# Kernel tuning notes

Measured on AMD Instinct MI355X. Metric: run time of the kernel, lower is better.

Reference implementation:

```python
import jax, jax.numpy as jnp
import numpy as np

N = 100000
H1, D1 = 8, 8          # conv1: 8 heads x 8 dims (concat -> 64)
C = 40                 # num_classes, conv2: 1 head
NEG_SLOPE = 0.2


def gat_layer(x, edge_index, W, a_src, a_dst, b, heads, out_dim, concat):
    # x: [N, F_in], W: [F_in, heads*out_dim], a_*: [heads, out_dim], b: [heads*out_dim] or [out_dim]
    h = (x @ W).reshape(-1, heads, out_dim)                 # [N, H, D]
    s_src = jnp.einsum('nhd,hd->nh', h, a_src)              # [N, H]
    s_dst = jnp.einsum('nhd,hd->nh', h, a_dst)              # [N, H]
    src, dst = edge_index[0], edge_index[1]
    e = jax.nn.leaky_relu(s_src[src] + s_dst[dst], NEG_SLOPE)   # [E, H]
    # segment softmax over incoming edges of each dst node
    m = jax.ops.segment_max(e, dst, num_segments=N)         # [N, H]
    e = jnp.exp(e - m[dst])
    z = jax.ops.segment_sum(e, dst, num_segments=N)         # [N, H]
    alpha = e / (z[dst] + 1e-16)                            # [E, H]
    msg = h[src] * alpha[:, :, None]                        # [E, H, D]
    out = jax.ops.segment_sum(msg, dst, num_segments=N)     # [N, H, D]
    if concat:
        out = out.reshape(-1, heads * out_dim)
    else:
        out = out.mean(axis=1)
    return out + b


def setup_inputs() -> dict:
    key = jax.random.key(0)
    ks = jax.random.split(key, 10)
    F_in = 256
    x = jax.random.normal(ks[0], (N, F_in), dtype=jnp.float32)
    edge_index = jax.random.randint(ks[1], (2, 1600000), 0, N, dtype=jnp.int32)
    sc1 = 1.0 / np.sqrt(F_in)
    W1 = jax.random.normal(ks[2], (F_in, H1 * D1), dtype=jnp.float32) * sc1
    a1_src = jax.random.normal(ks[3], (H1, D1), dtype=jnp.float32) * 0.1
    a1_dst = jax.random.normal(ks[4], (H1, D1), dtype=jnp.float32) * 0.1
    b1 = jnp.zeros((H1 * D1,), dtype=jnp.float32)
    sc2 = 1.0 / np.sqrt(H1 * D1)
    W2 = jax.random.normal(ks[5], (H1 * D1, C), dtype=jnp.float32) * sc2
    a2_src = jax.random.normal(ks[6], (1, C), dtype=jnp.float32) * 0.1
    a2_dst = jax.random.normal(ks[7], (1, C), dtype=jnp.float32) * 0.1
    b2 = jnp.zeros((C,), dtype=jnp.float32)
    return {"x": x, "edge_index": edge_index, "W1": W1, "a1_src": a1_src,
            "a1_dst": a1_dst, "b1": b1, "W2": W2, "a2_src": a2_src,
            "a2_dst": a2_dst, "b2": b2}


def reference(x, edge_index, W1, a1_src, a1_dst, b1, W2, a2_src, a2_dst, b2):
    # eval mode: dropout is identity
    h = gat_layer(x, edge_index, W1, a1_src, a1_dst, b1, H1, D1, concat=True)
    h = jax.nn.elu(h)
    out = gat_layer(h, edge_index, W2, a2_src, a2_dst, b2, 1, C, concat=False)
    return jax.nn.log_softmax(out, axis=1)
```

## Files before the change

### kernel.cpp

```cpp
#include <hip/hip_runtime.h>
#include <math.h>

#define BK 10
#define KNODES 1024
#define MAXNB 128

typedef __attribute__((ext_vector_type(8))) short bf16x8;
typedef __attribute__((ext_vector_type(4))) float f32x4;

__device__ __forceinline__ float bf2f(unsigned short u) {
  return __uint_as_float(((unsigned int)u) << 16);
}
__device__ __forceinline__ unsigned short f2bf(float f) {
  unsigned int i = __float_as_uint(f);
  unsigned int r = i + 0x7FFFu + ((i >> 16) & 1u);
  return (unsigned short)(r >> 16);
}

__global__ __launch_bounds__(256) void prep_kernel(
    const float* __restrict__ W1, const float* __restrict__ W2,
    const float* __restrict__ a2s, const float* __restrict__ a2d,
    unsigned short* __restrict__ whi, unsigned short* __restrict__ wlo,
    unsigned short* __restrict__ w2hi, unsigned short* __restrict__ w2lo,
    float* __restrict__ vas, float* __restrict__ vad,
    unsigned short* __restrict__ h1b, unsigned short* __restrict__ h2b,
    float* __restrict__ s1s, float* __restrict__ s2s,
    int* __restrict__ bpos, int capP, int NN) {
  const int blk = blockIdx.x, t = threadIdx.x;
  if (blk == 0 && t < MAXNB) bpos[t] = t * capP;
  if (blk < 32) {
    if (t < 64) {
      int b = blk, lane = t;
      int kt = b >> 2, ct = b & 3;
      int n = lane & 15, g = lane >> 4;
      unsigned short hb[8], lb[8];
#pragma unroll
      for (int j = 0; j < 8; ++j) {
        int k = kt * 32 + g * 8 + j;
        float wv = W1[k * 64 + ct * 16 + n];
        unsigned short hi = f2bf(wv);
        float rem = wv - bf2f(hi);
        hb[j] = hi;
        lb[j] = f2bf(rem);
      }
      size_t base = ((size_t)b * 64 + lane) * 8;
      *(ushort4*)(whi + base)     = make_ushort4(hb[0], hb[1], hb[2], hb[3]);
      *(ushort4*)(whi + base + 4) = make_ushort4(hb[4], hb[5], hb[6], hb[7]);
      *(ushort4*)(wlo + base)     = make_ushort4(lb[0], lb[1], lb[2], lb[3]);
      *(ushort4*)(wlo + base + 4) = make_ushort4(lb[4], lb[5], lb[6], lb[7]);
    }
  } else if (blk == 32) {
    if (t < 64) {
      float s = 0.f, d = 0.f;
      for (int c = 0; c < 40; ++c) {
        float w = W2[t * 40 + c];
        s += w * a2s[c];
        d += w * a2d[c];
      }
      vas[t] = s;
      vad[t] = d;
    }
  } else if (blk == 33) {
    if (t < 64) {
      h1b[(size_t)NN * 64 + t] = 0;
      if (t < 40) h2b[(size_t)NN * 40 + t] = 0;
      if (t < 8)  s1s[(size_t)NN * 8 + t] = -1e30f;
      if (t == 0) s2s[NN] = -1e30f;
    }
  } else if (blk >= 34 && blk < 40) {
    if (t < 64) {
      int b = blk - 34;
      int kt = b / 3, ct = b % 3;
      int n = t & 15, g = t >> 4;
      unsigned short hb[8], lb[8];
#pragma unroll
      for (int j = 0; j < 8; ++j) {
        int k = kt * 32 + g * 8 + j;
        int c = ct * 16 + n;
        float wv = (c < 40) ? W2[k * 40 + c] : 0.f;
        unsigned short hi = f2bf(wv);
        float rem = wv - bf2f(hi);
        hb[j] = hi;
        lb[j] = f2bf(rem);
      }
      size_t base = ((size_t)b * 64 + t) * 8;
      *(ushort4*)(w2hi + base)     = make_ushort4(hb[0], hb[1], hb[2], hb[3]);
      *(ushort4*)(w2hi + base + 4) = make_ushort4(hb[4], hb[5], hb[6], hb[7]);
      *(ushort4*)(w2lo + base)     = make_ushort4(lb[0], lb[1], lb[2], lb[3]);
      *(ushort4*)(w2lo + base + 4) = make_ushort4(lb[4], lb[5], lb[6], lb[7]);
    }
  }
}

__global__ __launch_bounds__(256) void gemm1_mfma_kernel(
    const float* __restrict__ x, const unsigned short* __restrict__ whi,
    const unsigned short* __restrict__ wlo,
    const float* __restrict__ a_src, const float* __restrict__ a_dst,
    unsigned short* __restrict__ h1b,
    float* __restrict__ s_src, float* __restrict__ s_dst, int N) {
  __shared__ float xtile[4][2048];
  const int w = threadIdx.x >> 6, lane = threadIdx.x & 63;
  const int m = lane & 15, g = lane >> 4;
  const int rbase = blockIdx.x * 64 + w * 16;
  float* xw = xtile[w];

  const int lrow2 = lane >> 5;
  const int lch   = lane & 31;
  const int msw   = m & 7;

  f32x4 acc[4] = {{0.f, 0.f, 0.f, 0.f}, {0.f, 0.f, 0.f, 0.f},
                  {0.f, 0.f, 0.f, 0.f}, {0.f, 0.f, 0.f, 0.f}};

#pragma unroll
  for (int half = 0; half < 2; ++half) {
    const int colbase = half * 128;
    if (half) asm volatile("s_waitcnt lgkmcnt(0)" ::: "memory");
#pragma unroll
    for (int j = 0; j < 8; ++j) {
      int lrow = 2 * j + lrow2;
      int row = rbase + lrow;
      if (row >= N) row = N - 1;
      int sw = lrow & 7;
      const float* src = x + (size_t)row * 256 + colbase + ((lch ^ sw) << 2);
      __builtin_amdgcn_global_load_lds(
          (const __attribute__((address_space(1))) unsigned int*)src,
          (__attribute__((address_space(3))) unsigned int*)(xw + j * 256),
          16, 0, 0);
    }
    asm volatile("s_waitcnt vmcnt(0)" ::: "memory");
#pragma unroll
    for (int ktl = 0; ktl < 4; ++ktl) {
      const int kt = half * 4 + ktl;
      const int c0 = ktl * 8 + g * 2;
      const float* p0 = xw + m * 128 + (((c0)     ^ msw) << 2);
      const float* p1 = xw + m * 128 + (((c0 + 1) ^ msw) << 2);
      float4 a0 = *(const float4*)p0;
      float4 a1 = *(const float4*)p1;
      float av[8] = {a0.x, a0.y, a0.z, a0.w, a1.x, a1.y, a1.z, a1.w};
      bf16x8 ahi, alo;
#pragma unroll
      for (int j = 0; j < 8; ++j) {
        unsigned int u = __float_as_uint(av[j]);
        unsigned short hi = (unsigned short)(u >> 16);
        float rem = av[j] - bf2f(hi);
        ahi[j] = (short)hi;
        alo[j] = (short)(__float_as_uint(rem) >> 16);
      }
      const unsigned short* wp = whi + ((size_t)(kt * 4) * 64 + lane) * 8;
      const unsigned short* lp = wlo + ((size_t)(kt * 4) * 64 + lane) * 8;
#pragma unroll
      for (int ct = 0; ct < 4; ++ct) {
        bf16x8 bh = *(const bf16x8*)(wp + (size_t)ct * 64 * 8);
        bf16x8 bl = *(const bf16x8*)(lp + (size_t)ct * 64 * 8);
        acc[ct] = __builtin_amdgcn_mfma_f32_16x16x32_bf16(ahi, bh, acc[ct], 0, 0, 0);
        acc[ct] = __builtin_amdgcn_mfma_f32_16x16x32_bf16(alo, bh, acc[ct], 0, 0, 0);
        acc[ct] = __builtin_amdgcn_mfma_f32_16x16x32_bf16(ahi, bl, acc[ct], 0, 0, 0);
      }
    }
  }
#pragma unroll
  for (int r = 0; r < 4; ++r) {
    int ro = rbase + g * 4 + r;
    if (ro < N) {
#pragma unroll
      for (int ct = 0; ct < 4; ++ct)
        h1b[(size_t)ro * 64 + ct * 16 + m] = f2bf(acc[ct][r]);
    }
  }
  float a1sv[4], a1dv[4];
#pragma unroll
  for (int ct = 0; ct < 4; ++ct) {
    a1sv[ct] = a_src[ct * 16 + m];
    a1dv[ct] = a_dst[ct * 16 + m];
  }
#pragma unroll
  for (int r = 0; r < 4; ++r) {
    float ps[4], pd[4];
#pragma unroll
    for (int ct = 0; ct < 4; ++ct) {
      ps[ct] = acc[ct][r] * a1sv[ct];
      pd[ct] = acc[ct][r] * a1dv[ct];
    }
#pragma unroll
    for (int off = 1; off < 8; off <<= 1) {
#pragma unroll
      for (int ct = 0; ct < 4; ++ct) {
        ps[ct] += __shfl_xor(ps[ct], off);
        pd[ct] += __shfl_xor(pd[ct], off);
      }
    }
    int ro = rbase + g * 4 + r;
    if ((m & 7) == 0 && ro < N) {
      int hb2 = m >> 3;
#pragma unroll
      for (int ct = 0; ct < 4; ++ct) {
        s_src[(size_t)ro * 8 + ct * 2 + hb2] = ps[ct];
        s_dst[(size_t)ro * 8 + ct * 2 + hb2] = pd[ct];
      }
    }
  }
}

__global__ __launch_bounds__(256) void bin_kernel(const int* __restrict__ src,
                                                  const int* __restrict__ dst,
                                                  int* __restrict__ bpos,
                                                  unsigned int* __restrict__ payload,
                                                  int E, int NB, int capP) {
  __shared__ int hist[MAXNB], soff[MAXNB], base[MAXNB], rnk[MAXNB];
  __shared__ unsigned int stage[4096];
  const int t = threadIdx.x;
  const int e0 = blockIdx.x * 4096;
  if (t < MAXNB) { hist[t] = 0; rnk[t] = 0; }
  __syncthreads();
  for (int j = t; j < 4096; j += 256) {
    int e = e0 + j;
    if (e < E) atomicAdd(&hist[dst[e] >> BK], 1);
  }
  __syncthreads();
  if (t == 0) {
    int acc = 0;
    for (int b = 0; b < NB; ++b) { soff[b] = acc; acc += hist[b]; }
  }
  __syncthreads();
  if (t < NB) {
    int c = hist[t];
    base[t] = c ? atomicAdd(&bpos[t], c) : 0;
  }
  __syncthreads();
  for (int j = t; j < 4096; j += 256) {
    int e = e0 + j;
    if (e < E) {
      int d = dst[e];
      int b = d >> BK;
      int s = src[e];
      int r = atomicAdd(&rnk[b], 1);
      stage[soff[b] + r] = (((unsigned)(d & (KNODES - 1))) << 17) | (unsigned)s;
    }
  }
  __syncthreads();
  int wave = t >> 6, lane = t & 63;
  for (int b = wave; b < NB; b += 4) {
    int len = hist[b], bs = soff[b], gb = base[b];
    int lim = (b + 1) * capP;
    for (int j = lane; j < len; j += 64)
      if (gb + j < lim) payload[gb + j] = stage[bs + j];
  }
}

__global__ __launch_bounds__(1024) void fill2_kernel(const unsigned int* __restrict__ payload,
                                                     const int* __restrict__ bpos,
                                                     int* __restrict__ col,
                                                     int* __restrict__ rbeg,
                                                     int* __restrict__ rend,
                                                     int capP, int NN) {
  __shared__ int cnt[KNODES], scn[KNODES], pos[KNODES];
  const int b = blockIdx.x, t = threadIdx.x;
  cnt[t] = 0;
  __syncthreads();
  const int beg = b * capP;
  int len = bpos[b] - beg;
  if (len > capP) len = capP;
  for (int j = t; j < len; j += 1024) atomicAdd(&cnt[payload[beg + j] >> 17], 1);
  __syncthreads();
  const int myc = cnt[t];
  const int padc = (myc + 7) & ~7;
  scn[t] = padc;
  __syncthreads();
  for (int off = 1; off < 1024; off <<= 1) {
    int v = (t >= off) ? scn[t - off] : 0;
    __syncthreads();
    scn[t] += v;
    __syncthreads();
  }
  const int mystart = b * (capP + 8 * KNODES) + scn[t] - padc;
  const int n = (b << BK) + t;
  if (n < NN) { rbeg[n] = mystart; rend[n] = mystart + padc; }
  pos[t] = mystart;
  __syncthreads();
  for (int j = t; j < len; j += 1024) {
    unsigned int pay = payload[beg + j];
    int p = atomicAdd(&pos[pay >> 17], 1);
    col[p] = (int)(pay & 0x1FFFF);
  }
  __syncthreads();
  for (int j = mystart + myc; j < mystart + padc; ++j) col[j] = NN;
}

__global__ __launch_bounds__(256) void agg1_kernel(
    const int* __restrict__ rbeg, const int* __restrict__ rend,
    const int* __restrict__ col,
    const float* __restrict__ s_src, const float* __restrict__ s_dst,
    const unsigned short* __restrict__ h1b, const float* __restrict__ b1,
    const float* __restrict__ vas, const float* __restrict__ vad,
    unsigned short* __restrict__ helub, float* __restrict__ s2s,
    float* __restrict__ s2d, int N) {
  int wv = threadIdx.x >> 6;
  int l  = threadIdx.x & 63;
  int n  = blockIdx.x * 4 + wv;
  if (n >= N) return;
  const int q  = l >> 3;
  const int hh = l & 7;
  const float sdq = s_dst[n * 8 + hh];
  const int beg = __builtin_amdgcn_readfirstlane(rbeg[n]);
  const int end = __builtin_amdgcn_readfirstlane(rend[n]);
  float z = 0.f, acc = 0.f, acc2 = 0.f;
  int e = beg;
  if (((end - beg) >> 3) & 1) {
    int4 ia = *(const int4*)(col + e);
    int4 ib = *(const int4*)(col + e + 4);
    int myidx = col[e + q];
    float pv = s_src[(unsigned)myidx * 8u + (unsigned)hh];
    float tt = pv + sdq;
    tt = fmaxf(tt, 0.2f * tt);
    float w = __expf(tt);
    z += w;
    int idxs[8] = {ia.x, ia.y, ia.z, ia.w, ib.x, ib.y, ib.z, ib.w};
#pragma unroll
    for (int j = 0; j < 8; ++j) {
      float wj = __shfl(w, j * 8 + q, 64);
      unsigned short g = h1b[(unsigned)idxs[j] * 64u + (unsigned)l];
      acc = fmaf(wj, bf2f(g), acc);
    }
    e += 8;
  }
  for (; e < end; e += 16) {
    int4 ia = *(const int4*)(col + e);
    int4 ib = *(const int4*)(col + e + 4);
    int4 ic = *(const int4*)(col + e + 8);
    int4 id = *(const int4*)(col + e + 12);
    int my0 = col[e + q];
    int my1 = col[e + 8 + q];
    float pv0 = s_src[(unsigned)my0 * 8u + (unsigned)hh];
    float pv1 = s_src[(unsigned)my1 * 8u + (unsigned)hh];
    int idxs[16] = {ia.x, ia.y, ia.z, ia.w, ib.x, ib.y, ib.z, ib.w,
                    ic.x, ic.y, ic.z, ic.w, id.x, id.y, id.z, id.w};
    unsigned short gg[16];
#pragma unroll
    for (int j = 0; j < 16; ++j) gg[j] = h1b[(unsigned)idxs[j] * 64u + (unsigned)l];
    float t0 = pv0 + sdq; t0 = fmaxf(t0, 0.2f * t0); float w0 = __expf(t0);
    float t1 = pv1 + sdq; t1 = fmaxf(t1, 0.2f * t1); float w1 = __expf(t1);
    z += w0 + w1;
#pragma unroll
    for (int j = 0; j < 8; ++j) {
      float wj = __shfl(w0, j * 8 + q, 64);
      acc = fmaf(wj, bf2f(gg[j]), acc);
    }
#pragma unroll
    for (int j = 0; j < 8; ++j) {
      float wj = __shfl(w1, j * 8 + q, 64);
      acc2 = fmaf(wj, bf2f(gg[8 + j]), acc2);
    }
  }
  acc += acc2;
  z += __shfl_xor(z, 8); z += __shfl_xor(z, 16); z += __shfl_xor(z, 32);
  float zf = __shfl(z, 9 * q, 64);
  float v = acc / (zf + 1e-16f) + b1[l];
  v = v > 0.f ? v : (__expf(v) - 1.f);
  helub[(size_t)n * 64 + l] = f2bf(v);
  float ps = v * vas[l];
  float pd = v * vad[l];
  for (int off = 32; off > 0; off >>= 1) {
    ps += __shfl_xor(ps, off);
    pd += __shfl_xor(pd, off);
  }
  if (l == 0) { s2s[n] = ps; s2d[n] = pd; }
}

__global__ __launch_bounds__(256) void gemm2_mfma_kernel(
    const unsigned short* __restrict__ heb, const unsigned short* __restrict__ w2hi,
    const unsigned short* __restrict__ w2lo, unsigned short* __restrict__ h2b, int N) {
  const int w = threadIdx.x >> 6, lane = threadIdx.x & 63;
  const int m = lane & 15, g = lane >> 4;
  const int rbase = blockIdx.x * 64 + w * 16;
  int arow = rbase + m;
  if (arow >= N) arow = N - 1;
  const unsigned short* hrow = heb + (size_t)arow * 64 + g * 8;
  f32x4 acc[3] = {{0.f, 0.f, 0.f, 0.f}, {0.f, 0.f, 0.f, 0.f}, {0.f, 0.f, 0.f, 0.f}};
#pragma unroll
  for (int kt = 0; kt < 2; ++kt) {
    bf16x8 a = *(const bf16x8*)(hrow + kt * 32);
#pragma unroll
    for (int ct = 0; ct < 3; ++ct) {
      int b = kt * 3 + ct;
      bf16x8 bh = *(const bf16x8*)(w2hi + ((size_t)b * 64 + lane) * 8);
      bf16x8 bl = *(const bf16x8*)(w2lo + ((size_t)b * 64 + lane) * 8);
      acc[ct] = __builtin_amdgcn_mfma_f32_16x16x32_bf16(a, bh, acc[ct], 0, 0, 0);
      acc[ct] = __builtin_amdgcn_mfma_f32_16x16x32_bf16(a, bl, acc[ct], 0, 0, 0);
    }
  }
#pragma unroll
  for (int r = 0; r < 4; ++r) {
    int ro = rbase + g * 4 + r;
    if (ro < N) {
#pragma unroll
      for (int ct = 0; ct < 3; ++ct) {
        int c = ct * 16 + m;
        if (c < 40) h2b[(size_t)ro * 40 + c] = f2bf(acc[ct][r]);
      }
    }
  }
}

__global__ __launch_bounds__(256) void agg2_kernel(
    const int* __restrict__ rbeg, const int* __restrict__ rend,
    const int* __restrict__ col,
    const float* __restrict__ s2s, const float* __restrict__ s2d,
    const unsigned short* __restrict__ h2b, const float* __restrict__ b2,
    float* __restrict__ out, int N) {
  int wv = threadIdx.x >> 6;
  int l  = threadIdx.x & 63;
  int n  = blockIdx.x * 4 + wv;
  if (n >= N) return;
  const int q = l >> 3;
  const bool act = (l < 40);
  const unsigned lc = act ? (unsigned)l : 0u;
  const float sdv = s2d[n];
  const int beg = __builtin_amdgcn_readfirstlane(rbeg[n]);
  const int end = __builtin_amdgcn_readfirstlane(rend[n]);
  float z = 0.f, acc = 0.f, acc2 = 0.f;
  int e = beg;
  if (((end - beg) >> 3) & 1) {
    int4 ia = *(const int4*)(col + e);
    int4 ib = *(const int4*)(col + e + 4);
    int myidx = col[e + q];
    float pv = s2s[myidx];
    float tt = pv + sdv;
    tt = fmaxf(tt, 0.2f * tt);
    float w = __expf(tt);
    z += w;
    int idxs[8] = {ia.x, ia.y, ia.z, ia.w, ib.x, ib.y, ib.z, ib.w};
#pragma unroll
    for (int j = 0; j < 8; ++j) {
      float wj = __shfl(w, j * 8, 64);
      unsigned short g = h2b[(unsigned)idxs[j] * 40u + lc];
      acc = fmaf(wj, bf2f(g), acc);
    }
    e += 8;
  }
  for (; e < end; e += 16) {
    int4 ia = *(const int4*)(col + e);
    int4 ib = *(const int4*)(col + e + 4);
    int4 ic = *(const int4*)(col + e + 8);
    int4 id = *(const int4*)(col + e + 12);
    int my0 = col[e + q];
    int my1 = col[e + 8 + q];
    float pv0 = s2s[my0];
    float pv1 = s2s[my1];
    int idxs[16] = {ia.x, ia.y, ia.z, ia.w, ib.x, ib.y, ib.z, ib.w,
                    ic.x, ic.y, ic.z, ic.w, id.x, id.y, id.z, id.w};
    unsigned short gg[16];
#pragma unroll
    for (int j = 0; j < 16; ++j) gg[j] = h2b[(unsigned)idxs[j] * 40u + lc];
    float t0 = pv0 + sdv; t0 = fmaxf(t0, 0.2f * t0); float w0 = __expf(t0);
    float t1 = pv1 + sdv; t1 = fmaxf(t1, 0.2f * t1); float w1 = __expf(t1);
    z += w0 + w1;
#pragma unroll
    for (int j = 0; j < 8; ++j) {
      float wj = __shfl(w0, j * 8, 64);
      acc = fmaf(wj, bf2f(gg[j]), acc);
    }
#pragma unroll
    for (int j = 0; j < 8; ++j) {
      float wj = __shfl(w1, j * 8, 64);
      acc2 = fmaf(wj, bf2f(gg[8 + j]), acc2);
    }
  }
  acc += acc2;
  z += __shfl_xor(z, 8); z += __shfl_xor(z, 16); z += __shfl_xor(z, 32);
  float v = act ? (acc / (z + 1e-16f) + b2[l]) : -1e30f;
  float m = v;
  for (int off = 32; off > 0; off >>= 1) m = fmaxf(m, __shfl_xor(m, off));
  float ex = act ? __expf(v - m) : 0.f;
  float s = ex;
  for (int off = 32; off > 0; off >>= 1) s += __shfl_xor(s, off);
  if (act) out[(size_t)n * 40 + l] = v - m - logf(s);
}

extern "C" void kernel_launch(void* const* d_in, const int* in_sizes, int n_in,
                              void* d_out, int out_size, void* d_ws, size_t ws_size,
                              hipStream_t stream) {
  const float* x   = (const float*)d_in[0];
  const int*   ei  = (const int*)d_in[1];
  const float* W1  = (const float*)d_in[2];
  const float* a1s = (const float*)d_in[3];
  const float* a1d = (const float*)d_in[4];
  const float* b1  = (const float*)d_in[5];
  const float* W2  = (const float*)d_in[6];
  const float* a2s = (const float*)d_in[7];
  const float* a2d = (const float*)d_in[8];
  const float* b2  = (const float*)d_in[9];
  float* out = (float*)d_out;
  (void)n_in; (void)out_size; (void)ws_size;

  const int NN = in_sizes[0] / 256;
  const int E  = in_sizes[1] / 2;
  const int NB = (NN + KNODES - 1) >> BK;
  const int* esrc = ei;
  const int* edst = ei + E;

  int capP = (E + NB - 1) / NB;
  capP += capP / 4 + capP / 16 + 512;
  capP = (capP + 15) & ~15;

  char* p = (char*)d_ws;
  auto alloc = [&](size_t bytes) -> char* {
    char* q = p;
    p += (bytes + 255) & ~(size_t)255;
    return q;
  };
  unsigned short* h1b   = (unsigned short*)alloc((size_t)(NN + 1) * 64 * 2);
  unsigned short* helub = (unsigned short*)alloc((size_t)NN * 64 * 2);
  unsigned short* h2b   = (unsigned short*)alloc((size_t)(NN + 1) * 40 * 2);
  float* s1s  = (float*)alloc((size_t)(NN + 1) * 8 * 4);
  float* s1d  = (float*)alloc((size_t)NN * 8 * 4);
  float* s2s  = (float*)alloc((size_t)(NN + 1) * 4);
  float* s2d  = (float*)alloc((size_t)NN * 4);
  int*   rbeg = (int*)alloc((size_t)NN * 4);
  int*   rend = (int*)alloc((size_t)NN * 4);
  int*   bpos = (int*)alloc(MAXNB * 4);
  unsigned int* payload = (unsigned int*)alloc((size_t)NB * capP * 4);
  int*   col  = (int*)alloc((size_t)NB * (capP + 8 * KNODES) * 4);
  float* vas  = (float*)alloc(64 * 4);
  float* vad  = (float*)alloc(64 * 4);
  unsigned short* w1hi = (unsigned short*)alloc(32 * 64 * 8 * 2);
  unsigned short* w1lo = (unsigned short*)alloc(32 * 64 * 8 * 2);
  unsigned short* w2hi = (unsigned short*)alloc(6 * 64 * 8 * 2);
  unsigned short* w2lo = (unsigned short*)alloc(6 * 64 * 8 * 2);

  prep_kernel<<<40, 256, 0, stream>>>(W1, W2, a2s, a2d, w1hi, w1lo, w2hi, w2lo,
                                      vas, vad, h1b, h2b, s1s, s2s, bpos, capP, NN);
  bin_kernel<<<(E + 4095) / 4096, 256, 0, stream>>>(esrc, edst, bpos, payload, E, NB, capP);
  fill2_kernel<<<NB, 1024, 0, stream>>>(payload, bpos, col, rbeg, rend, capP, NN);
  gemm1_mfma_kernel<<<(NN + 63) / 64, 256, 0, stream>>>(x, w1hi, w1lo, a1s, a1d,
                                                        h1b, s1s, s1d, NN);
  agg1_kernel<<<(NN + 3) / 4, 256, 0, stream>>>(rbeg, rend, col, s1s, s1d, h1b, b1,
                                                vas, vad, helub, s2s, s2d, NN);
  gemm2_mfma_kernel<<<(NN + 63) / 64, 256, 0, stream>>>(helub, w2hi, w2lo, h2b, NN);
  agg2_kernel<<<(NN + 3) / 4, 256, 0, stream>>>(rbeg, rend, col, s2s, s2d, h2b, b2, out, NN);
}
```

Before: 349.3 us.

## Fuse edge binning into GEMM1 launch and GEMM2 into layer-1 aggregation

Edge binning and the first-layer GEMM now run as one launch, with block roles interleaved and shared memory held in a union, so the two independent phases overlap on the device. The second-layer GEMM moves into the layer-1 aggregation kernel: each 512-thread block aggregates 8 nodes, stages the ELU outputs in LDS, and one wave runs the MFMA. This removes the helub intermediate round-trip through global memory and one launch. The fill kernel's block-wide Hillis-Steele scan is replaced by a wave-shuffle scan, cutting barriers. In exchange, only one wave per block does the MFMA work, on 8 of its 16 rows, and the larger blocks may lower occupancy in the aggregation kernel.

```diff
diff --git a/kernel.cpp b/kernel.cpp
--- a/kernel.cpp
+++ b/kernel.cpp
@@ -92,17 +92,79 @@
   }
 }
 
-__global__ __launch_bounds__(256) void gemm1_mfma_kernel(
+__global__ __launch_bounds__(256) void g1bin_kernel(
     const float* __restrict__ x, const unsigned short* __restrict__ whi,
     const unsigned short* __restrict__ wlo,
     const float* __restrict__ a_src, const float* __restrict__ a_dst,
     unsigned short* __restrict__ h1b,
-    float* __restrict__ s_src, float* __restrict__ s_dst, int N) {
-  __shared__ float xtile[4][2048];
+    float* __restrict__ s_src, float* __restrict__ s_dst, int N,
+    const int* __restrict__ esrc, const int* __restrict__ edst,
+    int* __restrict__ bpos, unsigned int* __restrict__ payload,
+    int E, int NB, int capP, int nG1, int nBin) {
+  __shared__ union {
+    float xtile[4][2048];
+    struct {
+      int hist[MAXNB], soff[MAXNB], base[MAXNB], rnk[MAXNB];
+      unsigned int stage[4096];
+    } b;
+  } sm;
+
+  const int bid = blockIdx.x;
+  int isBin, id;
+  if (2 * nBin <= nG1 + nBin) {
+    if (bid < 2 * nBin) { isBin = bid & 1; id = bid >> 1; }
+    else                { isBin = 0;       id = bid - nBin; }
+  } else {
+    isBin = (bid < nBin);
+    id = isBin ? bid : bid - nBin;
+  }
+
+  if (isBin) {
+    const int t = threadIdx.x;
+    const int e0 = id * 4096;
+    if (t < MAXNB) { sm.b.hist[t] = 0; sm.b.rnk[t] = 0; }
+    __syncthreads();
+    for (int j = t; j < 4096; j += 256) {
+      int e = e0 + j;
+      if (e < E) atomicAdd(&sm.b.hist[edst[e] >> BK], 1);
+    }
+    __syncthreads();
+    if (t == 0) {
+      int acc = 0;
+      for (int b = 0; b < NB; ++b) { sm.b.soff[b] = acc; acc += sm.b.hist[b]; }
+    }
+    __syncthreads();
+    if (t < NB) {
+      int c = sm.b.hist[t];
+      sm.b.base[t] = c ? atomicAdd(&bpos[t], c) : 0;
+    }
+    __syncthreads();
+    for (int j = t; j < 4096; j += 256) {
+      int e = e0 + j;
+      if (e < E) {
+        int d = edst[e];
+        int b = d >> BK;
+        int s = esrc[e];
+        int r = atomicAdd(&sm.b.rnk[b], 1);
+        sm.b.stage[sm.b.soff[b] + r] =
+            (((unsigned)(d & (KNODES - 1))) << 17) | (unsigned)s;
+      }
+    }
+    __syncthreads();
+    int wave = t >> 6, lane = t & 63;
+    for (int b = wave; b < NB; b += 4) {
+      int len = sm.b.hist[b], bs = sm.b.soff[b], gb = sm.b.base[b];
+      int lim = (b + 1) * capP;
+      for (int j = lane; j < len; j += 64)
+        if (gb + j < lim) payload[gb + j] = sm.b.stage[bs + j];
+    }
+    return;
+  }
+
   const int w = threadIdx.x >> 6, lane = threadIdx.x & 63;
   const int m = lane & 15, g = lane >> 4;
-  const int rbase = blockIdx.x * 64 + w * 16;
-  float* xw = xtile[w];
+  const int rbase = id * 64 + w * 16;
+  float* xw = sm.xtile[w];
 
   const int lrow2 = lane >> 5;
   const int lch   = lane & 31;
@@ -201,59 +263,14 @@
   }
 }
 
-__global__ __launch_bounds__(256) void bin_kernel(const int* __restrict__ src,
-                                                  const int* __restrict__ dst,
-                                                  int* __restrict__ bpos,
-                                                  unsigned int* __restrict__ payload,
-                                                  int E, int NB, int capP) {
-  __shared__ int hist[MAXNB], soff[MAXNB], base[MAXNB], rnk[MAXNB];
-  __shared__ unsigned int stage[4096];
-  const int t = threadIdx.x;
-  const int e0 = blockIdx.x * 4096;
-  if (t < MAXNB) { hist[t] = 0; rnk[t] = 0; }
-  __syncthreads();
-  for (int j = t; j < 4096; j += 256) {
-    int e = e0 + j;
-    if (e < E) atomicAdd(&hist[dst[e] >> BK], 1);
-  }
-  __syncthreads();
-  if (t == 0) {
-    int acc = 0;
-    for (int b = 0; b < NB; ++b) { soff[b] = acc; acc += hist[b]; }
-  }
-  __syncthreads();
-  if (t < NB) {
-    int c = hist[t];
-    base[t] = c ? atomicAdd(&bpos[t], c) : 0;
-  }
-  __syncthreads();
-  for (int j = t; j < 4096; j += 256) {
-    int e = e0 + j;
-    if (e < E) {
-      int d = dst[e];
-      int b = d >> BK;
-      int s = src[e];
-      int r = atomicAdd(&rnk[b], 1);
-      stage[soff[b] + r] = (((unsigned)(d & (KNODES - 1))) << 17) | (unsigned)s;
-    }
-  }
-  __syncthreads();
-  int wave = t >> 6, lane = t & 63;
-  for (int b = wave; b < NB; b += 4) {
-    int len = hist[b], bs = soff[b], gb = base[b];
-    int lim = (b + 1) * capP;
-    for (int j = lane; j < len; j += 64)
-      if (gb + j < lim) payload[gb + j] = stage[bs + j];
-  }
-}
-
 __global__ __launch_bounds__(1024) void fill2_kernel(const unsigned int* __restrict__ payload,
                                                      const int* __restrict__ bpos,
                                                      int* __restrict__ col,
                                                      int* __restrict__ rbeg,
                                                      int* __restrict__ rend,
                                                      int capP, int NN) {
-  __shared__ int cnt[KNODES], scn[KNODES], pos[KNODES];
+  __shared__ int cnt[KNODES], pos[KNODES];
+  __shared__ int wsum[16];
   const int b = blockIdx.x, t = threadIdx.x;
   cnt[t] = 0;
   __syncthreads();
@@ -264,15 +281,27 @@
   __syncthreads();
   const int myc = cnt[t];
   const int padc = (myc + 7) & ~7;
-  scn[t] = padc;
-  __syncthreads();
-  for (int off = 1; off < 1024; off <<= 1) {
-    int v = (t >= off) ? scn[t - off] : 0;
-    __syncthreads();
-    scn[t] += v;
-    __syncthreads();
-  }
-  const int mystart = b * (capP + 8 * KNODES) + scn[t] - padc;
+  const int lane = t & 63, wid = t >> 6;
+  int v = padc;
+#pragma unroll
+  for (int off = 1; off < 64; off <<= 1) {
+    int u = __shfl_up(v, off, 64);
+    if (lane >= off) v += u;
+  }
+  if (lane == 63) wsum[wid] = v;
+  __syncthreads();
+  if (t < 16) {
+    int sv = wsum[t];
+#pragma unroll
+    for (int off = 1; off < 16; off <<= 1) {
+      int u = __shfl_up(sv, off, 64);
+      if ((int)t >= off) sv += u;
+    }
+    wsum[t] = sv;
+  }
+  __syncthreads();
+  const int incl = v + (wid ? wsum[wid - 1] : 0);
+  const int mystart = b * (capP + 8 * KNODES) + incl - padc;
   const int n = (b << BK) + t;
   if (n < NN) { rbeg[n] = mystart; rend[n] = mystart + padc; }
   pos[t] = mystart;
@@ -286,116 +315,121 @@
   for (int j = mystart + myc; j < mystart + padc; ++j) col[j] = NN;
 }
 
-__global__ __launch_bounds__(256) void agg1_kernel(
+__global__ __launch_bounds__(512) void agg1_kernel(
     const int* __restrict__ rbeg, const int* __restrict__ rend,
     const int* __restrict__ col,
     const float* __restrict__ s_src, const float* __restrict__ s_dst,
     const unsigned short* __restrict__ h1b, const float* __restrict__ b1,
     const float* __restrict__ vas, const float* __restrict__ vad,
-    unsigned short* __restrict__ helub, float* __restrict__ s2s,
+    const unsigned short* __restrict__ w2hi, const unsigned short* __restrict__ w2lo,
+    unsigned short* __restrict__ h2b, float* __restrict__ s2s,
     float* __restrict__ s2d, int N) {
-  int wv = threadIdx.x >> 6;
-  int l  = threadIdx.x & 63;
-  int n  = blockIdx.x * 4 + wv;
-  if (n >= N) return;
-  const int q  = l >> 3;
-  const int hh = l & 7;
-  const float sdq = s_dst[n * 8 + hh];
-  const int beg = __builtin_amdgcn_readfirstlane(rbeg[n]);
-  const int end = __builtin_amdgcn_readfirstlane(rend[n]);
-  float z = 0.f, acc = 0.f, acc2 = 0.f;
-  int e = beg;
-  if (((end - beg) >> 3) & 1) {
-    int4 ia = *(const int4*)(col + e);
-    int4 ib = *(const int4*)(col + e + 4);
-    int myidx = col[e + q];
-    float pv = s_src[(unsigned)myidx * 8u + (unsigned)hh];
-    float tt = pv + sdq;
-    tt = fmaxf(tt, 0.2f * tt);
-    float w = __expf(tt);
-    z += w;
-    int idxs[8] = {ia.x, ia.y, ia.z, ia.w, ib.x, ib.y, ib.z, ib.w};
-#pragma unroll
-    for (int j = 0; j < 8; ++j) {
-      float wj = __shfl(w, j * 8 + q, 64);
-      unsigned short g = h1b[(unsigned)idxs[j] * 64u + (unsigned)l];
-      acc = fmaf(wj, bf2f(g), acc);
-    }
-    e += 8;
-  }
-  for (; e < end; e += 16) {
-    int4 ia = *(const int4*)(col + e);
-    int4 ib = *(const int4*)(col + e + 4);
-    int4 ic = *(const int4*)(col + e + 8);
-    int4 id = *(const int4*)(col + e + 12);
-    int my0 = col[e + q];
-    int my1 = col[e + 8 + q];
-    float pv0 = s_src[(unsigned)my0 * 8u + (unsigned)hh];
-    float pv1 = s_src[(unsigned)my1 * 8u + (unsigned)hh];
-    int idxs[16] = {ia.x, ia.y, ia.z, ia.w, ib.x, ib.y, ib.z, ib.w,
-                    ic.x, ic.y, ic.z, ic.w, id.x, id.y, id.z, id.w};
-    unsigned short gg[16];
-#pragma unroll
-    for (int j = 0; j < 16; ++j) gg[j] = h1b[(unsigned)idxs[j] * 64u + (unsigned)l];
-    float t0 = pv0 + sdq; t0 = fmaxf(t0, 0.2f * t0); float w0 = __expf(t0);
-    float t1 = pv1 + sdq; t1 = fmaxf(t1, 0.2f * t1); float w1 = __expf(t1);
-    z += w0 + w1;
-#pragma unroll
-    for (int j = 0; j < 8; ++j) {
-      float wj = __shfl(w0, j * 8 + q, 64);
-      acc = fmaf(wj, bf2f(gg[j]), acc);
-    }
-#pragma unroll
-    for (int j = 0; j < 8; ++j) {
-      float wj = __shfl(w1, j * 8 + q, 64);
-      acc2 = fmaf(wj, bf2f(gg[8 + j]), acc2);
-    }
-  }
-  acc += acc2;
-  z += __shfl_xor(z, 8); z += __shfl_xor(z, 16); z += __shfl_xor(z, 32);
-  float zf = __shfl(z, 9 * q, 64);
-  float v = acc / (zf + 1e-16f) + b1[l];
-  v = v > 0.f ? v : (__expf(v) - 1.f);
-  helub[(size_t)n * 64 + l] = f2bf(v);
-  float ps = v * vas[l];
-  float pd = v * vad[l];
-  for (int off = 32; off > 0; off >>= 1) {
-    ps += __shfl_xor(ps, off);
-    pd += __shfl_xor(pd, off);
-  }
-  if (l == 0) { s2s[n] = ps; s2d[n] = pd; }
-}
-
-__global__ __launch_bounds__(256) void gemm2_mfma_kernel(
-    const unsigned short* __restrict__ heb, const unsigned short* __restrict__ w2hi,
-    const unsigned short* __restrict__ w2lo, unsigned short* __restrict__ h2b, int N) {
-  const int w = threadIdx.x >> 6, lane = threadIdx.x & 63;
-  const int m = lane & 15, g = lane >> 4;
-  const int rbase = blockIdx.x * 64 + w * 16;
-  int arow = rbase + m;
-  if (arow >= N) arow = N - 1;
-  const unsigned short* hrow = heb + (size_t)arow * 64 + g * 8;
-  f32x4 acc[3] = {{0.f, 0.f, 0.f, 0.f}, {0.f, 0.f, 0.f, 0.f}, {0.f, 0.f, 0.f, 0.f}};
-#pragma unroll
-  for (int kt = 0; kt < 2; ++kt) {
-    bf16x8 a = *(const bf16x8*)(hrow + kt * 32);
-#pragma unroll
-    for (int ct = 0; ct < 3; ++ct) {
-      int b = kt * 3 + ct;
-      bf16x8 bh = *(const bf16x8*)(w2hi + ((size_t)b * 64 + lane) * 8);
-      bf16x8 bl = *(const bf16x8*)(w2lo + ((size_t)b * 64 + lane) * 8);
-      acc[ct] = __builtin_amdgcn_mfma_f32_16x16x32_bf16(a, bh, acc[ct], 0, 0, 0);
-      acc[ct] = __builtin_amdgcn_mfma_f32_16x16x32_bf16(a, bl, acc[ct], 0, 0, 0);
-    }
-  }
-#pragma unroll
-  for (int r = 0; r < 4; ++r) {
-    int ro = rbase + g * 4 + r;
-    if (ro < N) {
+  __shared__ float vsh[16][68];
+  const int t  = threadIdx.x;
+  const int wv = t >> 6;
+  const int l  = t & 63;
+  const int n  = blockIdx.x * 8 + wv;
+  const bool alive = (n < N);
+  float v = 0.f;
+  if (alive) {
+    const int q  = l >> 3;
+    const int hh = l & 7;
+    const float sdq = s_dst[n * 8 + hh];
+    const int beg = __builtin_amdgcn_readfirstlane(rbeg[n]);
+    const int end = __builtin_amdgcn_readfirstlane(rend[n]);
+    float z = 0.f, acc = 0.f, acc2 = 0.f;
+    int e = beg;
+    if (((end - beg) >> 3) & 1) {
+      int4 ia = *(const int4*)(col + e);
+      int4 ib = *(const int4*)(col + e + 4);
+      int myidx = col[e + q];
+      float pv = s_src[(unsigned)myidx * 8u + (unsigned)hh];
+      float tt = pv + sdq;
+      tt = fmaxf(tt, 0.2f * tt);
+      float ww = __expf(tt);
+      z += ww;
+      int idxs[8] = {ia.x, ia.y, ia.z, ia.w, ib.x, ib.y, ib.z, ib.w};
+#pragma unroll
+      for (int j = 0; j < 8; ++j) {
+        float wj = __shfl(ww, j * 8 + q, 64);
+        unsigned short gbit = h1b[(unsigned)idxs[j] * 64u + (unsigned)l];
+        acc = fmaf(wj, bf2f(gbit), acc);
+      }
+      e += 8;
+    }
+    for (; e < end; e += 16) {
+      int4 ia = *(const int4*)(col + e);
+      int4 ib = *(const int4*)(col + e + 4);
+      int4 ic = *(const int4*)(col + e + 8);
+      int4 id = *(const int4*)(col + e + 12);
+      int my0 = col[e + q];
+      int my1 = col[e + 8 + q];
+      float pv0 = s_src[(unsigned)my0 * 8u + (unsigned)hh];
+      float pv1 = s_src[(unsigned)my1 * 8u + (unsigned)hh];
+      int idxs[16] = {ia.x, ia.y, ia.z, ia.w, ib.x, ib.y, ib.z, ib.w,
+                      ic.x, ic.y, ic.z, ic.w, id.x, id.y, id.z, id.w};
+      unsigned short gg[16];
+#pragma unroll
+      for (int j = 0; j < 16; ++j) gg[j] = h1b[(unsigned)idxs[j] * 64u + (unsigned)l];
+      float t0 = pv0 + sdq; t0 = fmaxf(t0, 0.2f * t0); float w0 = __expf(t0);
+      float t1 = pv1 + sdq; t1 = fmaxf(t1, 0.2f * t1); float w1 = __expf(t1);
+      z += w0 + w1;
+#pragma unroll
+      for (int j = 0; j < 8; ++j) {
+        float wj = __shfl(w0, j * 8 + q, 64);
+        acc = fmaf(wj, bf2f(gg[j]), acc);
+      }
+#pragma unroll
+      for (int j = 0; j < 8; ++j) {
+        float wj = __shfl(w1, j * 8 + q, 64);
+        acc2 = fmaf(wj, bf2f(gg[8 + j]), acc2);
+      }
+    }
+    acc += acc2;
+    z += __shfl_xor(z, 8); z += __shfl_xor(z, 16); z += __shfl_xor(z, 32);
+    float zf = __shfl(z, 9 * q, 64);
+    v = acc / (zf + 1e-16f) + b1[l];
+    v = v > 0.f ? v : (__expf(v) - 1.f);
+    float ps = v * vas[l];
+    float pd = v * vad[l];
+    for (int off = 32; off > 0; off >>= 1) {
+      ps += __shfl_xor(ps, off);
+      pd += __shfl_xor(pd, off);
+    }
+    if (l == 0) { s2s[n] = ps; s2d[n] = pd; }
+  }
+  vsh[wv][l] = v;
+  __syncthreads();
+  if (wv == 0) {
+    const int m = l & 15, g = l >> 4;
+    const int rbase2 = blockIdx.x * 8;
+    f32x4 acc2t[3] = {{0.f, 0.f, 0.f, 0.f}, {0.f, 0.f, 0.f, 0.f},
+                      {0.f, 0.f, 0.f, 0.f}};
+#pragma unroll
+    for (int kt = 0; kt < 2; ++kt) {
+      bf16x8 a;
+#pragma unroll
+      for (int j = 0; j < 8; ++j)
+        a[j] = (short)f2bf(vsh[m][kt * 32 + g * 8 + j]);
 #pragma unroll
       for (int ct = 0; ct < 3; ++ct) {
-        int c = ct * 16 + m;
-        if (c < 40) h2b[(size_t)ro * 40 + c] = f2bf(acc[ct][r]);
+        int b = kt * 3 + ct;
+        bf16x8 bh = *(const bf16x8*)(w2hi + ((size_t)b * 64 + l) * 8);
+        bf16x8 bl = *(const bf16x8*)(w2lo + ((size_t)b * 64 + l) * 8);
+        acc2t[ct] = __builtin_amdgcn_mfma_f32_16x16x32_bf16(a, bh, acc2t[ct], 0, 0, 0);
+        acc2t[ct] = __builtin_amdgcn_mfma_f32_16x16x32_bf16(a, bl, acc2t[ct], 0, 0, 0);
+      }
+    }
+#pragma unroll
+    for (int r = 0; r < 4; ++r) {
+      int row = g * 4 + r;
+      int ro  = rbase2 + row;
+      if (row < 8 && ro < N) {
+#pragma unroll
+        for (int ct = 0; ct < 3; ++ct) {
+          int c = ct * 16 + m;
+          if (c < 40) h2b[(size_t)ro * 40 + c] = f2bf(acc2t[ct][r]);
+        }
       }
     }
   }
@@ -509,7 +543,6 @@
     return q;
   };
   unsigned short* h1b   = (unsigned short*)alloc((size_t)(NN + 1) * 64 * 2);
-  unsigned short* helub = (unsigned short*)alloc((size_t)NN * 64 * 2);
   unsigned short* h2b   = (unsigned short*)alloc((size_t)(NN + 1) * 40 * 2);
   float* s1s  = (float*)alloc((size_t)(NN + 1) * 8 * 4);
   float* s1d  = (float*)alloc((size_t)NN * 8 * 4);
@@ -527,14 +560,17 @@
   unsigned short* w2hi = (unsigned short*)alloc(6 * 64 * 8 * 2);
   unsigned short* w2lo = (unsigned short*)alloc(6 * 64 * 8 * 2);
 
+  const int nG1  = (NN + 63) / 64;
+  const int nBin = (E + 4095) / 4096;
+
   prep_kernel<<<40, 256, 0, stream>>>(W1, W2, a2s, a2d, w1hi, w1lo, w2hi, w2lo,
                                       vas, vad, h1b, h2b, s1s, s2s, bpos, capP, NN);
-  bin_kernel<<<(E + 4095) / 4096, 256, 0, stream>>>(esrc, edst, bpos, payload, E, NB, capP);
+  g1bin_kernel<<<nG1 + nBin, 256, 0, stream>>>(x, w1hi, w1lo, a1s, a1d, h1b,
+                                               s1s, s1d, NN, esrc, edst, bpos,
+                                               payload, E, NB, capP, nG1, nBin);
   fill2_kernel<<<NB, 1024, 0, stream>>>(payload, bpos, col, rbeg, rend, capP, NN);
-  gemm1_mfma_kernel<<<(NN + 63) / 64, 256, 0, stream>>>(x, w1hi, w1lo, a1s, a1d,
-                                                        h1b, s1s, s1d, NN);
-  agg1_kernel<<<(NN + 3) / 4, 256, 0, stream>>>(rbeg, rend, col, s1s, s1d, h1b, b1,
-                                                vas, vad, helub, s2s, s2d, NN);
-  gemm2_mfma_kernel<<<(NN + 63) / 64, 256, 0, stream>>>(helub, w2hi, w2lo, h2b, NN);
+  agg1_kernel<<<(NN + 7) / 8, 512, 0, stream>>>(rbeg, rend, col, s1s, s1d, h1b, b1,
+                                                vas, vad, w2hi, w2lo, h2b,
+                                                s2s, s2d, NN);
   agg2_kernel<<<(NN + 3) / 4, 256, 0, stream>>>(rbeg, rend, col, s2s, s2d, h2b, b2, out, NN);
 }
```

Measured after the change: 337.3 us. 1.04x faster.
